# Kernel tuning notes

Measured on AMD Instinct MI355X. Metric: run time of the kernel, lower is better.

The kernel has to match this reference:

```python
import jax, jax.numpy as jnp
import numpy as np

D_MODEL = 1024
N_HEADS = 16
HEAD_DIM = D_MODEL // N_HEADS
SCALE = HEAD_DIM ** -0.5


def setup_inputs() -> dict:
    key = jax.random.key(0)
    ks = jax.random.split(key, 5)
    B, T = 2, 2048
    w_std = D_MODEL ** -0.5  # ~ torch Linear init scale
    return {
        "x": jax.random.normal(ks[0], (B, T, D_MODEL), dtype=jnp.float32),
        "W_q": jax.random.normal(ks[1], (D_MODEL, D_MODEL), dtype=jnp.float32) * w_std,
        "W_k": jax.random.normal(ks[2], (D_MODEL, D_MODEL), dtype=jnp.float32) * w_std,
        "W_v": jax.random.normal(ks[3], (D_MODEL, D_MODEL), dtype=jnp.float32) * w_std,
        "W_o": jax.random.normal(ks[4], (D_MODEL, D_MODEL), dtype=jnp.float32) * w_std,
    }


def reference(x, W_q, W_k, W_v, W_o):
    # torch Linear: y = x @ W.T  (weight stored as (out, in))
    B, T, _ = x.shape

    def split_heads(y):  # (B,T,D) -> (B,H,T,hd)
        return y.reshape(B, T, N_HEADS, HEAD_DIM).transpose(0, 2, 1, 3)

    q = split_heads(x @ W_q.T)
    k = split_heads(x @ W_k.T)
    v = split_heads(x @ W_v.T)

    attn = jnp.einsum("bhqd,bhkd->bhqk", q, k) * SCALE  # (B,H,T,T)
    attn = jax.nn.softmax(attn, axis=-1)
    out = jnp.einsum("bhqk,bhkd->bhqd", attn, v)  # (B,H,T,hd)
    out = out.transpose(0, 2, 1, 3).reshape(B, T, D_MODEL)
    return out @ W_o.T
```

## Files before the change

### kernel.cpp

```cpp
#include <hip/hip_runtime.h>
#include <hip/hip_bf16.h>

#define D_MODEL 1024
#define N_HEADS 16
#define HEAD_DIM 64
#define SEQ 2048
#define BATCH 2

typedef __attribute__((ext_vector_type(8))) short bf16x8;
typedef __attribute__((ext_vector_type(4))) float f32x4;

typedef __attribute__((address_space(3))) unsigned lds_uint;
typedef __attribute__((address_space(1))) const unsigned global_cuint;

__device__ __forceinline__ void async_cp16(const ushort* g, ushort* l) {
  __builtin_amdgcn_global_load_lds((global_cuint*)g, (lds_uint*)l, 16, 0, 0);
}

__device__ __forceinline__ ushort f2b(float f) {
  union { float f; unsigned u; } x; x.f = f;
  unsigned r = x.u + 0x7fffu + ((x.u >> 16) & 1u);
  return (ushort)(r >> 16);
}

__device__ __forceinline__ unsigned pk2(float a, float b) {
  __hip_bfloat162 h = __float22bfloat162_rn(float2{a, b});
  union { __hip_bfloat162 h; unsigned u; } x; x.h = h;
  return x.u;
}

__device__ __forceinline__ float blo(unsigned u) {
  union { unsigned u; float f; } x; x.u = u << 16; return x.f;
}
__device__ __forceinline__ float bhi(unsigned u) {
  union { unsigned u; float f; } x; x.u = u & 0xffff0000u; return x.f;
}

__device__ __forceinline__ int swz64(int row, int colbyte) {
  return row * 64 + ((colbyte ^ ((row & 7) << 4)) >> 1);
}

__global__ __launch_bounds__(256) void cast_all(const float* __restrict__ x,
                                                const float* __restrict__ Wq,
                                                const float* __restrict__ Wk,
                                                const float* __restrict__ Wv,
                                                const float* __restrict__ Wo,
                                                ushort* __restrict__ xb,
                                                ushort* __restrict__ wqkv,
                                                ushort* __restrict__ wob) {
  int idx = blockIdx.x * 256 + threadIdx.x;
  const float* in;
  uint2* out;
  if (idx < (1 << 20)) {
    in = x; out = (uint2*)xb;
  } else {
    int j = idx - (1 << 20);
    int w = j >> 18;
    idx = j & 0x3FFFF;
    switch (w) {
      case 0: in = Wq; out = (uint2*)wqkv; break;
      case 1: in = Wk; out = (uint2*)(wqkv) + (1 << 18); break;
      case 2: in = Wv; out = (uint2*)(wqkv) + (2 << 18); break;
      default: in = Wo; out = (uint2*)wob; break;
    }
  }
  float4 v = ((const float4*)in)[idx];
  uint2 o; o.x = pk2(v.x, v.y); o.y = pk2(v.z, v.w);
  out[idx] = o;
}

__global__ __launch_bounds__(256) void gemm_qkv(const ushort* __restrict__ A,
                                                const ushort* __restrict__ Bw,
                                                ushort* __restrict__ Qh,
                                                ushort* __restrict__ Kh,
                                                ushort* __restrict__ Vth,
                                                float qscale) {
  constexpr int K = 1024;
  const int bm = blockIdx.y * 128;
  const int bn = blockIdx.x * 128;
  const int tid = threadIdx.x;
  const int wave = tid >> 6;
  const int lane = tid & 63;
  const int l16 = lane & 15;
  const int quad = lane >> 4;

  __shared__ ushort As[2][128 * 64];
  __shared__ ushort Bs[2][128 * 64];

  const int wm = (wave & 1) * 64;
  const int wn = (wave >> 1) * 64;

  f32x4 acc[4][4];
#pragma unroll
  for (int r = 0; r < 4; ++r)
#pragma unroll
    for (int c = 0; c < 4; ++c) acc[r][c] = (f32x4){0.f, 0.f, 0.f, 0.f};

  const int srow = wave * 8 + (lane >> 3);
  const int csw = (((lane & 7) ^ (lane >> 3)) << 3);

#pragma unroll
  for (int j = 0; j < 4; ++j) {
    async_cp16(A  + (size_t)(bm + j * 32 + srow) * K + csw, &As[0][(j * 32 + wave * 8) * 64]);
    async_cp16(Bw + (size_t)(bn + j * 32 + srow) * K + csw, &Bs[0][(j * 32 + wave * 8) * 64]);
  }

  constexpr int NIT = K / 64;
  for (int kt = 0; kt < NIT; ++kt) {
    __syncthreads();
    const int buf = kt & 1;
    if (kt + 1 < NIT) {
      const int k0 = (kt + 1) * 64;
#pragma unroll
      for (int j = 0; j < 4; ++j) {
        async_cp16(A  + (size_t)(bm + j * 32 + srow) * K + k0 + csw, &As[buf ^ 1][(j * 32 + wave * 8) * 64]);
        async_cp16(Bw + (size_t)(bn + j * 32 + srow) * K + k0 + csw, &Bs[buf ^ 1][(j * 32 + wave * 8) * 64]);
      }
    }

    bf16x8 a[2][4], b[2][4];
#pragma unroll
    for (int ks = 0; ks < 2; ++ks)
#pragma unroll
      for (int r = 0; r < 4; ++r) {
        a[ks][r] = *(const bf16x8*)(&As[buf][swz64(wm + r * 16 + l16, ks * 64 + quad * 16)]);
        b[ks][r] = *(const bf16x8*)(&Bs[buf][swz64(wn + r * 16 + l16, ks * 64 + quad * 16)]);
      }
#pragma unroll
    for (int ks = 0; ks < 2; ++ks)
#pragma unroll
      for (int r = 0; r < 4; ++r)
#pragma unroll
        for (int c = 0; c < 4; ++c)
          acc[r][c] = __builtin_amdgcn_mfma_f32_16x16x32_bf16(a[ks][r], b[ks][c], acc[r][c], 0, 0, 0);
  }

#pragma unroll
  for (int r = 0; r < 4; ++r) {
#pragma unroll
    for (int c = 0; c < 4; ++c) {
      int ncol = bn + wn + c * 16 + l16;
      int w = ncol >> 10;
      int f = ncol & 1023;
      int h = f >> 6, d = f & 63;
      if (w == 2) {
        int m0 = bm + wm + r * 16 + quad * 4;
        int b = m0 >> 11, t0 = m0 & 2047;
        uint2 pp;
        pp.x = pk2(acc[r][c][0], acc[r][c][1]);
        pp.y = pk2(acc[r][c][2], acc[r][c][3]);
        *(uint2*)(&Vth[((size_t)(b * 1024 + f) << 11) + t0]) = pp;
      } else {
#pragma unroll
        for (int rr = 0; rr < 4; ++rr) {
          float v = acc[r][c][rr];
          int m = bm + wm + r * 16 + quad * 4 + rr;
          int b = m >> 11, t = m & 2047;
          if (w == 0)
            Qh[((size_t)(b * 16 + h) * SEQ + t) * 64 + d] = f2b(v * qscale);
          else
            Kh[((size_t)(b * 16 + h) * SEQ + t) * 64 + d] = f2b(v);
        }
      }
    }
  }
}

__global__ __launch_bounds__(256) void gemm_out(const ushort* __restrict__ A,
                                                const ushort* __restrict__ Bw,
                                                float* __restrict__ out) {
  constexpr int K = 1024;
  const int bm = blockIdx.y * 64;
  const int bn = blockIdx.x * 128;
  const int tid = threadIdx.x;
  const int wave = tid >> 6;
  const int lane = tid & 63;
  const int l16 = lane & 15;
  const int quad = lane >> 4;

  __shared__ ushort As[2][64 * 64];
  __shared__ ushort Bs[2][128 * 64];

  const int wm = (wave & 1) * 32;
  const int wn = (wave >> 1) * 64;

  f32x4 acc[2][4];
#pragma unroll
  for (int r = 0; r < 2; ++r)
#pragma unroll
    for (int c = 0; c < 4; ++c) acc[r][c] = (f32x4){0.f, 0.f, 0.f, 0.f};

  const int srow = wave * 8 + (lane >> 3);
  const int csw = (((lane & 7) ^ (lane >> 3)) << 3);

#pragma unroll
  for (int j = 0; j < 2; ++j)
    async_cp16(A + (size_t)(bm + j * 32 + srow) * K + csw, &As[0][(j * 32 + wave * 8) * 64]);
#pragma unroll
  for (int j = 0; j < 4; ++j)
    async_cp16(Bw + (size_t)(bn + j * 32 + srow) * K + csw, &Bs[0][(j * 32 + wave * 8) * 64]);

  constexpr int NIT = K / 64;
  for (int kt = 0; kt < NIT; ++kt) {
    __syncthreads();
    const int buf = kt & 1;
    if (kt + 1 < NIT) {
      const int k0 = (kt + 1) * 64;
#pragma unroll
      for (int j = 0; j < 2; ++j)
        async_cp16(A + (size_t)(bm + j * 32 + srow) * K + k0 + csw, &As[buf ^ 1][(j * 32 + wave * 8) * 64]);
#pragma unroll
      for (int j = 0; j < 4; ++j)
        async_cp16(Bw + (size_t)(bn + j * 32 + srow) * K + k0 + csw, &Bs[buf ^ 1][(j * 32 + wave * 8) * 64]);
    }

    bf16x8 a[2][2], b[2][4];
#pragma unroll
    for (int ks = 0; ks < 2; ++ks) {
#pragma unroll
      for (int r = 0; r < 2; ++r)
        a[ks][r] = *(const bf16x8*)(&As[buf][swz64(wm + r * 16 + l16, ks * 64 + quad * 16)]);
#pragma unroll
      for (int c = 0; c < 4; ++c)
        b[ks][c] = *(const bf16x8*)(&Bs[buf][swz64(wn + c * 16 + l16, ks * 64 + quad * 16)]);
    }
#pragma unroll
    for (int ks = 0; ks < 2; ++ks)
#pragma unroll
      for (int r = 0; r < 2; ++r)
#pragma unroll
        for (int c = 0; c < 4; ++c)
          acc[r][c] = __builtin_amdgcn_mfma_f32_16x16x32_bf16(a[ks][r], b[ks][c], acc[r][c], 0, 0, 0);
  }

#pragma unroll
  for (int r = 0; r < 2; ++r)
#pragma unroll
    for (int c = 0; c < 4; ++c)
#pragma unroll
      for (int rr = 0; rr < 4; ++rr) {
        int m = bm + wm + r * 16 + quad * 4 + rr;
        int n = bn + wn + c * 16 + l16;
        out[(size_t)m * D_MODEL + n] = acc[r][c][rr];
      }
}

__global__ __launch_bounds__(256, 2) void attn_kernel(const ushort* __restrict__ Qh,
                                                      const ushort* __restrict__ Kh,
                                                      const ushort* __restrict__ Vth,
                                                      ushort* __restrict__ O1,
                                                      ushort* __restrict__ O2,
                                                      float* __restrict__ l1,
                                                      float* __restrict__ l2) {
  const int id = blockIdx.x;
  const int stream = id & 63;
  const int qb = id >> 6;
  const int bh = stream >> 1;
  const int half = stream & 1;
  const int q0 = qb * 128;
  ushort* __restrict__ Op = half ? O2 : O1;
  float* __restrict__ lp = half ? l2 : l1;

  const int tid = threadIdx.x;
  const int wave = tid >> 6;
  const int lane = tid & 63;
  const int l16 = lane & 15;
  const int quad = lane >> 4;

  __shared__ ushort KVbuf[2][2][64 * 64];
  __shared__ ushort Pt[64 * 64];

  bf16x8 qf[2][2];
#pragma unroll
  for (int g = 0; g < 2; ++g) {
    const ushort* qp = Qh + ((size_t)bh * SEQ + q0 + wave * 32 + g * 16 + l16) * 64 + quad * 8;
    qf[g][0] = *(const bf16x8*)(qp);
    qf[g][1] = *(const bf16x8*)(qp + 32);
  }

  f32x4 o[2][4];
  float lacc[2] = {0.f, 0.f};
#pragma unroll
  for (int g = 0; g < 2; ++g)
#pragma unroll
    for (int c = 0; c < 4; ++c) o[g][c] = (f32x4){0.f, 0.f, 0.f, 0.f};

  const int chunk = wave * 2;
  const int r8 = lane >> 3;
  const int csw = (((lane & 7) ^ r8) << 3);
  const ushort* kbase = Kh + ((size_t)bh * SEQ + half * 1024) * 64;
  const ushort* vbase = Vth + (size_t)bh * 64 * SEQ + half * 1024;
  const ushort* ksrc = kbase + (size_t)(chunk * 8 + r8) * 64 + csw;
  const ushort* vsrc = vbase + (size_t)(chunk * 8 + r8) * SEQ + csw;

  async_cp16(ksrc,           &KVbuf[0][0][chunk * 512]);
  async_cp16(ksrc + 8 * 64,  &KVbuf[0][0][(chunk + 1) * 512]);
  async_cp16(vsrc,           &KVbuf[0][1][chunk * 512]);
  async_cp16(vsrc + 8 * SEQ, &KVbuf[0][1][(chunk + 1) * 512]);

  constexpr int NIT = 1024 / 64;
  for (int kt = 0; kt < NIT; ++kt) {
    __syncthreads();
    const int buf = kt & 1;
    if (kt + 1 < NIT) {
      const ushort* ks = ksrc + (size_t)(kt + 1) * 64 * 64;
      const ushort* vs = vsrc + (kt + 1) * 64;
      async_cp16(ks,           &KVbuf[buf ^ 1][0][chunk * 512]);
      async_cp16(ks + 8 * 64,  &KVbuf[buf ^ 1][0][(chunk + 1) * 512]);
      async_cp16(vs,           &KVbuf[buf ^ 1][1][chunk * 512]);
      async_cp16(vs + 8 * SEQ, &KVbuf[buf ^ 1][1][(chunk + 1) * 512]);
    }
    const ushort* Kt = KVbuf[buf][0];
    const ushort* Vt = KVbuf[buf][1];
    const int prow = wave * 16 + l16;

    bf16x8 pf[2][2];
#pragma unroll
    for (int g = 0; g < 2; ++g) {
#pragma unroll
      for (int c = 0; c < 4; ++c) {
        bf16x8 ka0 = *(const bf16x8*)(&Kt[swz64(c * 16 + l16, quad * 16)]);
        bf16x8 ka1 = *(const bf16x8*)(&Kt[swz64(c * 16 + l16, 64 + quad * 16)]);
        f32x4 z = (f32x4){0.f, 0.f, 0.f, 0.f};
        z = __builtin_amdgcn_mfma_f32_16x16x32_bf16(ka0, qf[g][0], z, 0, 0, 0);
        z = __builtin_amdgcn_mfma_f32_16x16x32_bf16(ka1, qf[g][1], z, 0, 0, 0);
        float e0 = __builtin_amdgcn_exp2f(z[0]);
        float e1 = __builtin_amdgcn_exp2f(z[1]);
        float e2 = __builtin_amdgcn_exp2f(z[2]);
        float e3 = __builtin_amdgcn_exp2f(z[3]);
        lacc[g] += (e0 + e1) + (e2 + e3);
        uint2 pp;
        pp.x = pk2(e0, e1);
        pp.y = pk2(e2, e3);
        *(uint2*)(&Pt[swz64(prow, c * 32 + quad * 8)]) = pp;
      }
      pf[g][0] = *(const bf16x8*)(&Pt[swz64(prow, quad * 16)]);
      pf[g][1] = *(const bf16x8*)(&Pt[swz64(prow, 64 + quad * 16)]);
    }

#pragma unroll
    for (int c = 0; c < 4; ++c) {
      bf16x8 vb0 = *(const bf16x8*)(&Vt[swz64(c * 16 + l16, quad * 16)]);
      bf16x8 vb1 = *(const bf16x8*)(&Vt[swz64(c * 16 + l16, 64 + quad * 16)]);
#pragma unroll
      for (int g = 0; g < 2; ++g) {
        o[g][c] = __builtin_amdgcn_mfma_f32_16x16x32_bf16(pf[g][0], vb0, o[g][c], 0, 0, 0);
        o[g][c] = __builtin_amdgcn_mfma_f32_16x16x32_bf16(pf[g][1], vb1, o[g][c], 0, 0, 0);
      }
    }
  }

#pragma unroll
  for (int g = 0; g < 2; ++g) {
    lacc[g] += __shfl_xor(lacc[g], 16, 64);
    lacc[g] += __shfl_xor(lacc[g], 32, 64);
    if (quad == 0)
      lp[(size_t)bh * SEQ + q0 + wave * 32 + g * 16 + l16] = lacc[g];
  }

  __syncthreads();
  ushort* Ob = &KVbuf[0][0][0];
#pragma unroll
  for (int g = 0; g < 2; ++g)
#pragma unroll
    for (int r = 0; r < 4; ++r) {
      int row = wave * 32 + g * 16 + quad * 4 + r;
#pragma unroll
      for (int c = 0; c < 4; ++c)
        Ob[row * 64 + c * 16 + l16] = f2b(o[g][c][r]);
    }
  __syncthreads();
  {
    uint4* dst = (uint4*)(Op + ((size_t)bh * SEQ + q0) * 64);
    const uint4* src = (const uint4*)Ob;
#pragma unroll
    for (int i = 0; i < 4; ++i)
      dst[i * 256 + tid] = src[i * 256 + tid];
  }
}

__global__ __launch_bounds__(256) void recombine(const ushort* __restrict__ O1,
                                                 const ushort* __restrict__ O2,
                                                 const float* __restrict__ l1,
                                                 const float* __restrict__ l2,
                                                 ushort* __restrict__ ctx) {
  int idx = blockIdx.x * 256 + threadIdx.x;
  int row = idx >> 3;
  int d8 = idx & 7;
  uint4 a = ((const uint4*)O1)[idx];
  uint4 b = ((const uint4*)O2)[idx];
  float linv = 1.f / (l1[row] + l2[row]);
  uint4 res;
  unsigned* ap = (unsigned*)&a;
  unsigned* bp = (unsigned*)&b;
  unsigned* rp = (unsigned*)&res;
#pragma unroll
  for (int i = 0; i < 4; ++i) {
    float lo = (blo(ap[i]) + blo(bp[i])) * linv;
    float hi = (bhi(ap[i]) + bhi(bp[i])) * linv;
    rp[i] = pk2(lo, hi);
  }
  int bh = row >> 11, t = row & 2047;
  int bb = bh >> 4, h = bh & 15;
  ((uint4*)ctx)[(size_t)(bb * SEQ + t) * 128 + h * 8 + d8] = res;
}

extern "C" void kernel_launch(void* const* d_in, const int* in_sizes, int n_in,
                              void* d_out, int out_size, void* d_ws, size_t ws_size,
                              hipStream_t stream) {
  const float* x  = (const float*)d_in[0];
  const float* Wq = (const float*)d_in[1];
  const float* Wk = (const float*)d_in[2];
  const float* Wv = (const float*)d_in[3];
  const float* Wo = (const float*)d_in[4];
  float* out = (float*)d_out;

  char* ws = (char*)d_ws;
  const size_t MB = 1 << 20;
  ushort* xb   = (ushort*)(ws);
  ushort* wqkv = (ushort*)(ws +  8 * MB);
  ushort* wob  = (ushort*)(ws + 14 * MB);
  ushort* Qh   = (ushort*)(ws + 16 * MB);
  ushort* Kh   = (ushort*)(ws + 24 * MB);
  ushort* Vth  = (ushort*)(ws + 32 * MB);
  ushort* ctx  = (ushort*)(ws + 40 * MB);

  ushort* O1 = (ushort*)d_out;
  ushort* O2 = xb;
  float*  l1 = (float*)wqkv;
  float*  l2 = (float*)(ws + 8 * MB + 256 * 1024);

  cast_all<<<8192, 256, 0, stream>>>(x, Wq, Wk, Wv, Wo, xb, wqkv, wob);

  const float qscale = 0.125f * 1.44269504089f;
  gemm_qkv<<<dim3(3072 / 128, 4096 / 128), 256, 0, stream>>>(xb, wqkv, Qh, Kh, Vth, qscale);

  attn_kernel<<<(SEQ / 128) * BATCH * N_HEADS * 2, 256, 0, stream>>>(
      Qh, Kh, Vth, O1, O2, l1, l2);

  recombine<<<(BATCH * N_HEADS * SEQ * 64 / 8) / 256, 256, 0, stream>>>(O1, O2, l1, l2, ctx);

  gemm_out<<<dim3(1024 / 128, 4096 / 64), 256, 0, stream>>>(ctx, wob, out);
}
```

Baseline: 198.9 us.

## Switch attention kernel to 32x32x16 MFMA with register-resident P via lane shuffles

Rewrites the attention inner loop to use 32x32x16 bf16 MFMA instead of 16x16x32, with each wave owning 32 query rows. The exponentiated scores are packed into bf16 and rearranged between lane halves with xor-32 shuffles, so they can feed the PV MFMA straight from registers. This drops the LDS round-trip through the Pt scratch buffer, along with its stores and reloads. In exchange it adds shuffles and selects, raises accumulator register pressure, and changes the output write-back layout.

New measurement: 200.8 us. No clear change (+0.9%).

```diff
diff --git a/kernel.cpp b/kernel.cpp
--- a/kernel.cpp
+++ b/kernel.cpp
@@ -9,6 +9,7 @@
 
 typedef __attribute__((ext_vector_type(8))) short bf16x8;
 typedef __attribute__((ext_vector_type(4))) float f32x4;
+typedef __attribute__((ext_vector_type(16))) float f32x16;
 
 typedef __attribute__((address_space(3))) unsigned lds_uint;
 typedef __attribute__((address_space(1))) const unsigned global_cuint;
@@ -264,26 +265,20 @@
   const int tid = threadIdx.x;
   const int wave = tid >> 6;
   const int lane = tid & 63;
-  const int l16 = lane & 15;
-  const int quad = lane >> 4;
+  const int l31 = lane & 31;
+  const int hi = lane >> 5;
 
   __shared__ ushort KVbuf[2][2][64 * 64];
-  __shared__ ushort Pt[64 * 64];
-
-  bf16x8 qf[2][2];
-#pragma unroll
-  for (int g = 0; g < 2; ++g) {
-    const ushort* qp = Qh + ((size_t)bh * SEQ + q0 + wave * 32 + g * 16 + l16) * 64 + quad * 8;
-    qf[g][0] = *(const bf16x8*)(qp);
-    qf[g][1] = *(const bf16x8*)(qp + 32);
-  }
-
-  f32x4 o[2][4];
-  float lacc[2] = {0.f, 0.f};
-#pragma unroll
-  for (int g = 0; g < 2; ++g)
-#pragma unroll
-    for (int c = 0; c < 4; ++c) o[g][c] = (f32x4){0.f, 0.f, 0.f, 0.f};
+
+  bf16x8 qf[4];
+#pragma unroll
+  for (int dc = 0; dc < 4; ++dc)
+    qf[dc] = *(const bf16x8*)(Qh + ((size_t)bh * SEQ + q0 + wave * 32 + l31) * 64 + dc * 16 + hi * 8);
+
+  f32x16 o0 = {0.f, 0.f, 0.f, 0.f, 0.f, 0.f, 0.f, 0.f,
+               0.f, 0.f, 0.f, 0.f, 0.f, 0.f, 0.f, 0.f};
+  f32x16 o1 = o0;
+  float lacc = 0.f;
 
   const int chunk = wave * 2;
   const int r8 = lane >> 3;
@@ -312,63 +307,66 @@
     }
     const ushort* Kt = KVbuf[buf][0];
     const ushort* Vt = KVbuf[buf][1];
-    const int prow = wave * 16 + l16;
-
-    bf16x8 pf[2][2];
-#pragma unroll
-    for (int g = 0; g < 2; ++g) {
-#pragma unroll
-      for (int c = 0; c < 4; ++c) {
-        bf16x8 ka0 = *(const bf16x8*)(&Kt[swz64(c * 16 + l16, quad * 16)]);
-        bf16x8 ka1 = *(const bf16x8*)(&Kt[swz64(c * 16 + l16, 64 + quad * 16)]);
-        f32x4 z = (f32x4){0.f, 0.f, 0.f, 0.f};
-        z = __builtin_amdgcn_mfma_f32_16x16x32_bf16(ka0, qf[g][0], z, 0, 0, 0);
-        z = __builtin_amdgcn_mfma_f32_16x16x32_bf16(ka1, qf[g][1], z, 0, 0, 0);
-        float e0 = __builtin_amdgcn_exp2f(z[0]);
-        float e1 = __builtin_amdgcn_exp2f(z[1]);
-        float e2 = __builtin_amdgcn_exp2f(z[2]);
-        float e3 = __builtin_amdgcn_exp2f(z[3]);
-        lacc[g] += (e0 + e1) + (e2 + e3);
-        uint2 pp;
-        pp.x = pk2(e0, e1);
-        pp.y = pk2(e2, e3);
-        *(uint2*)(&Pt[swz64(prow, c * 32 + quad * 8)]) = pp;
+
+#pragma unroll
+    for (int kt2 = 0; kt2 < 2; ++kt2) {
+      bf16x8 ka0 = *(const bf16x8*)(&Kt[swz64(kt2 * 32 + l31, 0 * 32 + hi * 16)]);
+      bf16x8 ka1 = *(const bf16x8*)(&Kt[swz64(kt2 * 32 + l31, 1 * 32 + hi * 16)]);
+      bf16x8 ka2 = *(const bf16x8*)(&Kt[swz64(kt2 * 32 + l31, 2 * 32 + hi * 16)]);
+      bf16x8 ka3 = *(const bf16x8*)(&Kt[swz64(kt2 * 32 + l31, 3 * 32 + hi * 16)]);
+      f32x16 z = {0.f, 0.f, 0.f, 0.f, 0.f, 0.f, 0.f, 0.f,
+                  0.f, 0.f, 0.f, 0.f, 0.f, 0.f, 0.f, 0.f};
+      z = __builtin_amdgcn_mfma_f32_32x32x16_bf16(ka0, qf[0], z, 0, 0, 0);
+      z = __builtin_amdgcn_mfma_f32_32x32x16_bf16(ka1, qf[1], z, 0, 0, 0);
+      z = __builtin_amdgcn_mfma_f32_32x32x16_bf16(ka2, qf[2], z, 0, 0, 0);
+      z = __builtin_amdgcn_mfma_f32_32x32x16_bf16(ka3, qf[3], z, 0, 0, 0);
+
+      float e[16];
+#pragma unroll
+      for (int r = 0; r < 16; ++r) e[r] = __builtin_amdgcn_exp2f(z[r]);
+      lacc += (((e[0] + e[1]) + (e[2] + e[3])) + ((e[4] + e[5]) + (e[6] + e[7])))
+            + (((e[8] + e[9]) + (e[10] + e[11])) + ((e[12] + e[13]) + (e[14] + e[15])));
+
+#pragma unroll
+      for (int lw = 0; lw < 2; ++lw) {
+        const int base = lw * 8;
+        unsigned pa0 = pk2(e[base + 0], e[base + 1]);
+        unsigned pa1 = pk2(e[base + 2], e[base + 3]);
+        unsigned pa2 = pk2(e[base + 4], e[base + 5]);
+        unsigned pa3 = pk2(e[base + 6], e[base + 7]);
+        unsigned s0 = hi ? pa0 : pa2;
+        unsigned s1 = hi ? pa1 : pa3;
+        unsigned t0 = __shfl_xor(s0, 32, 64);
+        unsigned t1 = __shfl_xor(s1, 32, 64);
+        pa2 = hi ? pa2 : t0;
+        pa3 = hi ? pa3 : t1;
+        pa0 = hi ? t0 : pa0;
+        pa1 = hi ? t1 : pa1;
+        union { unsigned u[4]; bf16x8 v; } pu;
+        pu.u[0] = pa0; pu.u[1] = pa1; pu.u[2] = pa2; pu.u[3] = pa3;
+        const int wb = (kt2 * 2 + lw) * 32;
+        bf16x8 vb0 = *(const bf16x8*)(&Vt[swz64(0 + l31, wb + hi * 16)]);
+        bf16x8 vb1 = *(const bf16x8*)(&Vt[swz64(32 + l31, wb + hi * 16)]);
+        o0 = __builtin_amdgcn_mfma_f32_32x32x16_bf16(pu.v, vb0, o0, 0, 0, 0);
+        o1 = __builtin_amdgcn_mfma_f32_32x32x16_bf16(pu.v, vb1, o1, 0, 0, 0);
       }
-      pf[g][0] = *(const bf16x8*)(&Pt[swz64(prow, quad * 16)]);
-      pf[g][1] = *(const bf16x8*)(&Pt[swz64(prow, 64 + quad * 16)]);
-    }
-
-#pragma unroll
-    for (int c = 0; c < 4; ++c) {
-      bf16x8 vb0 = *(const bf16x8*)(&Vt[swz64(c * 16 + l16, quad * 16)]);
-      bf16x8 vb1 = *(const bf16x8*)(&Vt[swz64(c * 16 + l16, 64 + quad * 16)]);
-#pragma unroll
-      for (int g = 0; g < 2; ++g) {
-        o[g][c] = __builtin_amdgcn_mfma_f32_16x16x32_bf16(pf[g][0], vb0, o[g][c], 0, 0, 0);
-        o[g][c] = __builtin_amdgcn_mfma_f32_16x16x32_bf16(pf[g][1], vb1, o[g][c], 0, 0, 0);
-      }
-    }
-  }
-
-#pragma unroll
-  for (int g = 0; g < 2; ++g) {
-    lacc[g] += __shfl_xor(lacc[g], 16, 64);
-    lacc[g] += __shfl_xor(lacc[g], 32, 64);
-    if (quad == 0)
-      lp[(size_t)bh * SEQ + q0 + wave * 32 + g * 16 + l16] = lacc[g];
+    }
+  }
+
+  {
+    float ltot = lacc + __shfl_xor(lacc, 32, 64);
+    if (hi == 0)
+      lp[(size_t)bh * SEQ + q0 + wave * 32 + l31] = ltot;
   }
 
   __syncthreads();
   ushort* Ob = &KVbuf[0][0][0];
 #pragma unroll
-  for (int g = 0; g < 2; ++g)
-#pragma unroll
-    for (int r = 0; r < 4; ++r) {
-      int row = wave * 32 + g * 16 + quad * 4 + r;
-#pragma unroll
-      for (int c = 0; c < 4; ++c)
-        Ob[row * 64 + c * 16 + l16] = f2b(o[g][c][r]);
-    }
+  for (int r = 0; r < 16; ++r) {
+    int row = wave * 32 + (r & 3) + 8 * (r >> 2) + 4 * hi;
+    Ob[row * 64 + l31] = f2b(o0[r]);
+    Ob[row * 64 + 32 + l31] = f2b(o1[r]);
+  }
   __syncthreads();
   {
     uint4* dst = (uint4*)(Op + ((size_t)bh * SEQ + q0) * 64);
```
